# Optimization experiments

Hardware: AMD Instinct MI355X
Metric: run time of the kernel (lower is better)

The kernel has to match this reference:

```python
import jax, jax.numpy as jnp
import numpy as np

B, T, C, H = 2, 2048, 1024, 16
HD = C // H  # 64

def setup_inputs() -> dict:
    key = jax.random.key(0)
    ks = jax.random.split(key, 9)
    s = 0.02
    return {
        "x": jax.random.normal(ks[0], (B, T, C), jnp.float32),
        "Wq": jax.random.normal(ks[1], (C, C), jnp.float32) * s,
        "bq": jax.random.normal(ks[2], (C,), jnp.float32) * s,
        "Wk": jax.random.normal(ks[3], (C, C), jnp.float32) * s,
        "bk": jax.random.normal(ks[4], (C,), jnp.float32) * s,
        "Wv": jax.random.normal(ks[5], (C, C), jnp.float32) * s,
        "bv": jax.random.normal(ks[6], (C,), jnp.float32) * s,
        "Wp": jax.random.normal(ks[7], (C, C), jnp.float32) * s,
        "bp": jax.random.normal(ks[8], (C,), jnp.float32) * s,
    }

def reference(x, Wq, bq, Wk, bk, Wv, bv, Wp, bp):
    Bb, Tt, Cc = x.shape
    hd = Cc // H
    # project and split heads: [B, H, T, hd]
    def heads(W, b):
        return (x @ W.T + b).reshape(Bb, Tt, H, hd).transpose(0, 2, 1, 3)
    q, k, v = heads(Wq, bq), heads(Wk, bk), heads(Wv, bv)
    scale = 1.0 / np.sqrt(hd).astype(np.float32)
    att = jnp.einsum('bhqd,bhkd->bhqk', q, k) * scale
    causal = jnp.tril(jnp.ones((Tt, Tt), bool))
    att = jnp.where(causal[None, None], att, -jnp.inf)
    att = jax.nn.softmax(att, axis=-1)
    y = jnp.einsum('bhqk,bhkd->bhqd', att, v)
    y = y.transpose(0, 2, 1, 3).reshape(Bb, Tt, Cc)
    return y @ Wp.T + bp
```

## Files before the change

### kernel.cpp

```cpp
#include <hip/hip_runtime.h>
#include <hip/hip_bf16.h>

#define Tsz 2048
#define Csz 1024
#define Hn 16

typedef short s8v __attribute__((ext_vector_type(8)));
typedef short s4v __attribute__((ext_vector_type(4)));
typedef float f4v __attribute__((ext_vector_type(4)));

#define QSCALE (0.125f * 1.44269504088896f)

__device__ __forceinline__ short bf_bits(float x) {
    __hip_bfloat16 t = __float2bfloat16(x);
    return *reinterpret_cast<short*>(&t);
}

__device__ __forceinline__ void gload_lds(const void* g, void* l) {
    __builtin_amdgcn_global_load_lds(
        (const __attribute__((address_space(1))) void*)g,
        (__attribute__((address_space(3))) void*)l, 16, 0, 0);
}

__global__ void cvt5(const float* __restrict__ x, const float* __restrict__ wq,
                     const float* __restrict__ wk, const float* __restrict__ wv,
                     const float* __restrict__ wp,
                     short* __restrict__ xo, short* __restrict__ qo,
                     short* __restrict__ ko, short* __restrict__ vo,
                     short* __restrict__ po) {
    const int y = blockIdx.y;
    const float* in; short* out; int n;
    switch (y) {
        case 0: in = x;  out = xo; n = 2 * Tsz * Csz; break;
        case 1: in = wq; out = qo; n = Csz * Csz; break;
        case 2: in = wk; out = ko; n = Csz * Csz; break;
        case 3: in = wv; out = vo; n = Csz * Csz; break;
        default: in = wp; out = po; n = Csz * Csz; break;
    }
    int i = (blockIdx.x * blockDim.x + threadIdx.x) * 4;
    if (i >= n) return;
    float4 v = *(const float4*)(in + i);
    short4 o;
    o.x = bf_bits(v.x); o.y = bf_bits(v.y); o.z = bf_bits(v.z); o.w = bf_bits(v.w);
    *(short4*)(out + i) = o;
}

__global__ __launch_bounds__(256, 2) void qkv_gemm(
    const short* __restrict__ X,
    const short* __restrict__ Wq, const short* __restrict__ Wk, const short* __restrict__ Wv,
    const float* __restrict__ bq, const float* __restrict__ bk, const float* __restrict__ bv,
    short* __restrict__ Qo, short* __restrict__ Ko, short* __restrict__ Vto)
{
    const int z = blockIdx.z;
    const short* W = (z == 0) ? Wq : (z == 1) ? Wk : Wv;
    const float* bias = (z == 0) ? bq : (z == 1) ? bk : bv;

    __shared__ __align__(16) short Ash[128 * 32];
    __shared__ __align__(16) short Bsh[128 * 32];

    const int tid = threadIdx.x, lane = tid & 63, wave = tid >> 6;
    const int ln = lane & 15, hi = lane >> 4;
    const int m0 = blockIdx.x * 128, n0 = blockIdx.y * 128;
    const int wm = (wave >> 1) * 64, wn = (wave & 1) * 64;

    const short* Ag = X + (size_t)(m0 + (tid >> 2)) * Csz + (tid & 3) * 8;
    const short* Bg = W + (size_t)(n0 + (tid >> 2)) * Csz + (tid & 3) * 8;

    f4v acc[4][4];
    #pragma unroll
    for (int mt = 0; mt < 4; mt++)
        #pragma unroll
        for (int nt = 0; nt < 4; nt++)
            #pragma unroll
            for (int i = 0; i < 4; i++) acc[mt][nt][i] = 0.f;

    for (int k0 = 0; k0 < Csz; k0 += 32) {
        __syncthreads();
        gload_lds(Ag + k0, Ash + tid * 8);
        gload_lds(Ag + k0 + (size_t)64 * Csz, Ash + 2048 + tid * 8);
        gload_lds(Bg + k0, Bsh + tid * 8);
        gload_lds(Bg + k0 + (size_t)64 * Csz, Bsh + 2048 + tid * 8);
        __syncthreads();

        s8v af[4], bfr[4];
        #pragma unroll
        for (int mt = 0; mt < 4; mt++)
            af[mt] = *(const s8v*)(Ash + (wm + mt * 16 + ln) * 32 + hi * 8);
        #pragma unroll
        for (int nt = 0; nt < 4; nt++)
            bfr[nt] = *(const s8v*)(Bsh + (wn + nt * 16 + ln) * 32 + hi * 8);
        #pragma unroll
        for (int mt = 0; mt < 4; mt++)
            #pragma unroll
            for (int nt = 0; nt < 4; nt++)
                acc[mt][nt] = __builtin_amdgcn_mfma_f32_16x16x32_bf16(af[mt], bfr[nt], acc[mt][nt], 0, 0, 0);
    }

    const float scale = (z == 0) ? QSCALE : 1.0f;
    short* out = (z == 0) ? Qo : Ko;

    #pragma unroll
    for (int nt = 0; nt < 4; nt++) {
        const int col = n0 + wn + nt * 16 + ln;
        const float bvv = bias[col];
        #pragma unroll
        for (int mt = 0; mt < 4; mt++) {
            const int row0 = m0 + wm + mt * 16 + hi * 4;
            if (z == 2) {
                const int b = row0 >> 11, t = row0 & 2047;
                s4v pk;
                #pragma unroll
                for (int i = 0; i < 4; i++) pk[i] = bf_bits(acc[mt][nt][i] + bvv);
                *(s4v*)(Vto + (size_t)(b * 1024 + col) * Tsz + t) = pk;
            } else {
                #pragma unroll
                for (int i = 0; i < 4; i++)
                    out[(size_t)(row0 + i) * Csz + col] = bf_bits((acc[mt][nt][i] + bvv) * scale);
            }
        }
    }
}

__global__ __launch_bounds__(256, 2) void proj_gemm(
    const short* __restrict__ A, const short* __restrict__ W,
    const float* __restrict__ bias, float* __restrict__ out)
{
    __shared__ __align__(16) short Ash[128 * 32];
    __shared__ __align__(16) short Bsh[128 * 32];

    const int tid = threadIdx.x, lane = tid & 63, wave = tid >> 6;
    const int ln = lane & 15, hi = lane >> 4;
    const int m0 = blockIdx.x * 128, n0 = blockIdx.y * 128;
    const int wm = (wave >> 1) * 64, wn = (wave & 1) * 64;

    const short* Ag = A + (size_t)(m0 + (tid >> 2)) * Csz + (tid & 3) * 8;
    const short* Bg = W + (size_t)(n0 + (tid >> 2)) * Csz + (tid & 3) * 8;

    f4v acc[4][4];
    #pragma unroll
    for (int mt = 0; mt < 4; mt++)
        #pragma unroll
        for (int nt = 0; nt < 4; nt++)
            #pragma unroll
            for (int i = 0; i < 4; i++) acc[mt][nt][i] = 0.f;

    for (int k0 = 0; k0 < Csz; k0 += 32) {
        __syncthreads();
        gload_lds(Ag + k0, Ash + tid * 8);
        gload_lds(Ag + k0 + (size_t)64 * Csz, Ash + 2048 + tid * 8);
        gload_lds(Bg + k0, Bsh + tid * 8);
        gload_lds(Bg + k0 + (size_t)64 * Csz, Bsh + 2048 + tid * 8);
        __syncthreads();

        s8v af[4], bfr[4];
        #pragma unroll
        for (int mt = 0; mt < 4; mt++)
            af[mt] = *(const s8v*)(Ash + (wm + mt * 16 + ln) * 32 + hi * 8);
        #pragma unroll
        for (int nt = 0; nt < 4; nt++)
            bfr[nt] = *(const s8v*)(Bsh + (wn + nt * 16 + ln) * 32 + hi * 8);
        #pragma unroll
        for (int mt = 0; mt < 4; mt++)
            #pragma unroll
            for (int nt = 0; nt < 4; nt++)
                acc[mt][nt] = __builtin_amdgcn_mfma_f32_16x16x32_bf16(af[mt], bfr[nt], acc[mt][nt], 0, 0, 0);
    }

    #pragma unroll
    for (int nt = 0; nt < 4; nt++) {
        const int col = n0 + wn + nt * 16 + ln;
        const float bvv = bias[col];
        #pragma unroll
        for (int mt = 0; mt < 4; mt++)
            #pragma unroll
            for (int i = 0; i < 4; i++)
                out[(size_t)(m0 + wm + mt * 16 + hi * 4 + i) * Csz + col] = acc[mt][nt][i] + bvv;
    }
}

__global__ __launch_bounds__(256, 2) void attn4(
    const short* __restrict__ Q, const short* __restrict__ Kg,
    const short* __restrict__ Vt, short* __restrict__ Y)
{
    __shared__ __align__(16) short Ksh[64 * 72];
    __shared__ __align__(16) short Vsh[64 * 72];
    __shared__ __align__(16) short Psh[4][16 * 72];

    const int tid = threadIdx.x, lane = tid & 63, wave = tid >> 6;
    const int ln = lane & 15, hi = lane >> 4;
    const int p = blockIdx.x;
    const int qts[2] = { p, 31 - p };
    const int bh = blockIdx.y;
    const size_t base = (size_t)(bh >> 4) * Tsz * Csz + (size_t)(bh & 15) * 64;
    const size_t vtbase = (size_t)bh * 64 * Tsz;
    const int qrel = wave * 16 + ln;
    short* Pq = Psh[wave];

    s8v qf[2][2];
    #pragma unroll
    for (int t = 0; t < 2; t++)
        #pragma unroll
        for (int kk = 0; kk < 2; kk++)
            qf[t][kk] = *(const s8v*)(Q + base + (size_t)(qts[t] * 64 + qrel) * Csz + kk * 32 + hi * 8);

    f4v o[2][4], lacc[2];
    #pragma unroll
    for (int t = 0; t < 2; t++) {
        #pragma unroll
        for (int i = 0; i < 4; i++) lacc[t][i] = 0.f;
        #pragma unroll
        for (int dt = 0; dt < 4; dt++)
            #pragma unroll
            for (int i = 0; i < 4; i++) o[t][dt][i] = 0.f;
    }

    s8v ones;
    #pragma unroll
    for (int j = 0; j < 8; j++) ones[j] = (short)0x3F80;

    const int sr = tid >> 2, sc = (tid & 3) * 16;
    const short* Kp = Kg + base + (size_t)sr * Csz + sc;
    const short* Vp = Vt + vtbase + (size_t)sr * Tsz + sc;
    short* KshW = Ksh + sr * 72 + sc;
    short* VshW = Vsh + sr * 72 + sc;

    const int nkb = qts[1] + 1;
    for (int kb = 0; kb < nkb; kb++) {
        const int k0 = kb * 64;
        const s8v ka = *(const s8v*)(Kp + (size_t)k0 * Csz);
        const s8v kb2 = *(const s8v*)(Kp + (size_t)k0 * Csz + 8);
        const s8v va = *(const s8v*)(Vp + k0);
        const s8v vb2 = *(const s8v*)(Vp + k0 + 8);
        __syncthreads();
        *(s8v*)(KshW) = ka; *(s8v*)(KshW + 8) = kb2;
        *(s8v*)(VshW) = va; *(s8v*)(VshW + 8) = vb2;
        __syncthreads();

        s8v kf[2][4], vf[2][4];
        #pragma unroll
        for (int nt = 0; nt < 4; nt++)
            #pragma unroll
            for (int kk = 0; kk < 2; kk++) {
                kf[kk][nt] = *(const s8v*)(Ksh + (nt * 16 + ln) * 72 + kk * 32 + hi * 8);
                vf[kk][nt] = *(const s8v*)(Vsh + (nt * 16 + ln) * 72 + kk * 32 + hi * 8);
            }

        #pragma unroll
        for (int t = 0; t < 2; t++) {
            if (t == 0 && kb > qts[0]) continue;
            const bool dg = (kb == qts[t]);

            f4v s[4];
            #pragma unroll
            for (int nt = 0; nt < 4; nt++) {
                #pragma unroll
                for (int i = 0; i < 4; i++) s[nt][i] = 0.f;
                s[nt] = __builtin_amdgcn_mfma_f32_16x16x32_bf16(kf[0][nt], qf[t][0], s[nt], 0, 0, 0);
                s[nt] = __builtin_amdgcn_mfma_f32_16x16x32_bf16(kf[1][nt], qf[t][1], s[nt], 0, 0, 0);
            }

            #pragma unroll
            for (int nt = 0; nt < 4; nt++) {
                float pv[4];
                #pragma unroll
                for (int i = 0; i < 4; i++) pv[i] = exp2f(s[nt][i]);
                if (dg) {
                    const int kr = nt * 16 + hi * 4;
                    #pragma unroll
                    for (int i = 0; i < 4; i++)
                        if (kr + i > qrel) pv[i] = 0.f;
                }
                s4v w;
                #pragma unroll
                for (int i = 0; i < 4; i++) w[i] = bf_bits(pv[i]);
                *(s4v*)(Pq + ln * 72 + nt * 16 + hi * 4) = w;
            }
            const s8v pb0 = *(const s8v*)(Pq + ln * 72 + hi * 8);
            const s8v pb1 = *(const s8v*)(Pq + ln * 72 + 32 + hi * 8);

            #pragma unroll
            for (int dt = 0; dt < 4; dt++) {
                o[t][dt] = __builtin_amdgcn_mfma_f32_16x16x32_bf16(vf[0][dt], pb0, o[t][dt], 0, 0, 0);
                o[t][dt] = __builtin_amdgcn_mfma_f32_16x16x32_bf16(vf[1][dt], pb1, o[t][dt], 0, 0, 0);
            }
            lacc[t] = __builtin_amdgcn_mfma_f32_16x16x32_bf16(ones, pb0, lacc[t], 0, 0, 0);
            lacc[t] = __builtin_amdgcn_mfma_f32_16x16x32_bf16(ones, pb1, lacc[t], 0, 0, 0);
        }
    }

    #pragma unroll
    for (int t = 0; t < 2; t++) {
        const float inv = 1.0f / lacc[t][0];
        const int qrow = qts[t] * 64 + qrel;
        #pragma unroll
        for (int dt = 0; dt < 4; dt++) {
            s4v w;
            #pragma unroll
            for (int i = 0; i < 4; i++) w[i] = bf_bits(o[t][dt][i] * inv);
            *(s4v*)(Y + base + (size_t)qrow * Csz + dt * 16 + hi * 4) = w;
        }
    }
}

extern "C" void kernel_launch(void* const* d_in, const int* in_sizes, int n_in,
                              void* d_out, int out_size, void* d_ws, size_t ws_size,
                              hipStream_t stream) {
    const float* x  = (const float*)d_in[0];
    const float* Wq = (const float*)d_in[1];
    const float* bq = (const float*)d_in[2];
    const float* Wk = (const float*)d_in[3];
    const float* bk = (const float*)d_in[4];
    const float* Wv = (const float*)d_in[5];
    const float* bv = (const float*)d_in[6];
    const float* Wp = (const float*)d_in[7];
    const float* bp = (const float*)d_in[8];

    char* ws = (char*)d_ws;
    short* Xb  = (short*)(ws);
    short* Wqb = (short*)(ws + (8u  << 20));
    short* Wkb = (short*)(ws + (10u << 20));
    short* Wvb = (short*)(ws + (12u << 20));
    short* Wpb = (short*)(ws + (14u << 20));
    short* Qb  = (short*)(ws + (16u << 20));
    short* Kb  = (short*)(ws + (24u << 20));
    short* Vtb = (short*)(ws + (32u << 20));
    short* Yb  = (short*)(ws + (40u << 20));

    hipLaunchKernelGGL(cvt5, dim3(4096, 5), dim3(256), 0, stream,
                       x, Wq, Wk, Wv, Wp, Xb, Wqb, Wkb, Wvb, Wpb);

    hipLaunchKernelGGL(qkv_gemm, dim3(32, 8, 3), dim3(256), 0, stream,
                       Xb, Wqb, Wkb, Wvb, bq, bk, bv, Qb, Kb, Vtb);

    hipLaunchKernelGGL(attn4, dim3(16, 32), dim3(256), 0, stream, Qb, Kb, Vtb, Yb);

    hipLaunchKernelGGL(proj_gemm, dim3(32, 8), dim3(256), 0, stream, Yb, Wpb, bp, (float*)d_out);
}
```

Baseline: 190.4 us.

## Coalesce V-transpose stores, prefetch K/V in attention, shrink proj tiles

The QKV GEMM now stages its V output through an LDS transpose buffer so the transposed V is written as wide coalesced 16-element runs instead of scattered 4-element stores. Its launch bound is raised to 3 blocks per CU. The attention kernel register-prefetches the next K/V tile while computing the current one. It also replaces the row-sum MFMAs against a ones vector with scalar accumulation plus cross-lane shuffles. The projection GEMM uses 128x64 tiles to double the grid for better CU fill, which costs more A reloads and extra LDS and register pressure.

```diff
diff --git a/kernel.cpp b/kernel.cpp
--- a/kernel.cpp
+++ b/kernel.cpp
@@ -45,7 +45,7 @@
     *(short4*)(out + i) = o;
 }
 
-__global__ __launch_bounds__(256, 2) void qkv_gemm(
+__global__ __launch_bounds__(256, 3) void qkv_gemm(
     const short* __restrict__ X,
     const short* __restrict__ Wq, const short* __restrict__ Wk, const short* __restrict__ Wv,
     const float* __restrict__ bq, const float* __restrict__ bk, const float* __restrict__ bv,
@@ -57,6 +57,7 @@
 
     __shared__ __align__(16) short Ash[128 * 32];
     __shared__ __align__(16) short Bsh[128 * 32];
+    __shared__ __align__(16) short TR[64 * 72];
 
     const int tid = threadIdx.x, lane = tid & 63, wave = tid >> 6;
     const int ln = lane & 15, hi = lane >> 4;
@@ -96,6 +97,37 @@
                 acc[mt][nt] = __builtin_amdgcn_mfma_f32_16x16x32_bf16(af[mt], bfr[nt], acc[mt][nt], 0, 0, 0);
     }
 
+    if (z == 2) {
+        const int b = m0 >> 11, t0 = m0 & 2047;
+        float bvv[4];
+        #pragma unroll
+        for (int nt = 0; nt < 4; nt++) bvv[nt] = bias[n0 + wn + nt * 16 + ln];
+        #pragma unroll
+        for (int ph = 0; ph < 4; ph++) {
+            const int mh = ph >> 1, nh = ph & 1;
+            __syncthreads();
+            if ((wave >> 1) == mh && (wave & 1) == nh) {
+                #pragma unroll
+                for (int mt = 0; mt < 4; mt++)
+                    #pragma unroll
+                    for (int nt = 0; nt < 4; nt++) {
+                        s4v pk;
+                        #pragma unroll
+                        for (int i = 0; i < 4; i++) pk[i] = bf_bits(acc[mt][nt][i] + bvv[nt]);
+                        *(s4v*)(TR + (nt * 16 + ln) * 72 + mt * 16 + hi * 4) = pk;
+                    }
+            }
+            __syncthreads();
+            const int chl = tid >> 2, seg = tid & 3;
+            const s8v r0 = *(const s8v*)(TR + chl * 72 + seg * 16);
+            const s8v r1 = *(const s8v*)(TR + chl * 72 + seg * 16 + 8);
+            short* dst = Vto + (size_t)(b * 1024 + n0 + nh * 64 + chl) * Tsz + t0 + mh * 64 + seg * 16;
+            *(s8v*)(dst) = r0;
+            *(s8v*)(dst + 8) = r1;
+        }
+        return;
+    }
+
     const float scale = (z == 0) ? QSCALE : 1.0f;
     short* out = (z == 0) ? Qo : Ko;
 
@@ -106,17 +138,9 @@
         #pragma unroll
         for (int mt = 0; mt < 4; mt++) {
             const int row0 = m0 + wm + mt * 16 + hi * 4;
-            if (z == 2) {
-                const int b = row0 >> 11, t = row0 & 2047;
-                s4v pk;
-                #pragma unroll
-                for (int i = 0; i < 4; i++) pk[i] = bf_bits(acc[mt][nt][i] + bvv);
-                *(s4v*)(Vto + (size_t)(b * 1024 + col) * Tsz + t) = pk;
-            } else {
-                #pragma unroll
-                for (int i = 0; i < 4; i++)
-                    out[(size_t)(row0 + i) * Csz + col] = bf_bits((acc[mt][nt][i] + bvv) * scale);
-            }
+            #pragma unroll
+            for (int i = 0; i < 4; i++)
+                out[(size_t)(row0 + i) * Csz + col] = bf_bits((acc[mt][nt][i] + bvv) * scale);
         }
     }
 }
@@ -126,21 +150,21 @@
     const float* __restrict__ bias, float* __restrict__ out)
 {
     __shared__ __align__(16) short Ash[128 * 32];
-    __shared__ __align__(16) short Bsh[128 * 32];
+    __shared__ __align__(16) short Bsh[64 * 32];
 
     const int tid = threadIdx.x, lane = tid & 63, wave = tid >> 6;
     const int ln = lane & 15, hi = lane >> 4;
-    const int m0 = blockIdx.x * 128, n0 = blockIdx.y * 128;
-    const int wm = (wave >> 1) * 64, wn = (wave & 1) * 64;
+    const int m0 = blockIdx.x * 128, n0 = blockIdx.y * 64;
+    const int wm = (wave >> 1) * 64, wn = (wave & 1) * 32;
 
     const short* Ag = A + (size_t)(m0 + (tid >> 2)) * Csz + (tid & 3) * 8;
     const short* Bg = W + (size_t)(n0 + (tid >> 2)) * Csz + (tid & 3) * 8;
 
-    f4v acc[4][4];
+    f4v acc[4][2];
     #pragma unroll
     for (int mt = 0; mt < 4; mt++)
         #pragma unroll
-        for (int nt = 0; nt < 4; nt++)
+        for (int nt = 0; nt < 2; nt++)
             #pragma unroll
             for (int i = 0; i < 4; i++) acc[mt][nt][i] = 0.f;
 
@@ -149,25 +173,24 @@
         gload_lds(Ag + k0, Ash + tid * 8);
         gload_lds(Ag + k0 + (size_t)64 * Csz, Ash + 2048 + tid * 8);
         gload_lds(Bg + k0, Bsh + tid * 8);
-        gload_lds(Bg + k0 + (size_t)64 * Csz, Bsh + 2048 + tid * 8);
-        __syncthreads();
-
-        s8v af[4], bfr[4];
+        __syncthreads();
+
+        s8v af[4], bfr[2];
         #pragma unroll
         for (int mt = 0; mt < 4; mt++)
             af[mt] = *(const s8v*)(Ash + (wm + mt * 16 + ln) * 32 + hi * 8);
         #pragma unroll
-        for (int nt = 0; nt < 4; nt++)
+        for (int nt = 0; nt < 2; nt++)
             bfr[nt] = *(const s8v*)(Bsh + (wn + nt * 16 + ln) * 32 + hi * 8);
         #pragma unroll
         for (int mt = 0; mt < 4; mt++)
             #pragma unroll
-            for (int nt = 0; nt < 4; nt++)
+            for (int nt = 0; nt < 2; nt++)
                 acc[mt][nt] = __builtin_amdgcn_mfma_f32_16x16x32_bf16(af[mt], bfr[nt], acc[mt][nt], 0, 0, 0);
     }
 
     #pragma unroll
-    for (int nt = 0; nt < 4; nt++) {
+    for (int nt = 0; nt < 2; nt++) {
         const int col = n0 + wn + nt * 16 + ln;
         const float bvv = bias[col];
         #pragma unroll
@@ -178,7 +201,7 @@
     }
 }
 
-__global__ __launch_bounds__(256, 2) void attn4(
+__global__ __launch_bounds__(256, 2) void attn6(
     const short* __restrict__ Q, const short* __restrict__ Kg,
     const short* __restrict__ Vt, short* __restrict__ Y)
 {
@@ -203,20 +226,14 @@
         for (int kk = 0; kk < 2; kk++)
             qf[t][kk] = *(const s8v*)(Q + base + (size_t)(qts[t] * 64 + qrel) * Csz + kk * 32 + hi * 8);
 
-    f4v o[2][4], lacc[2];
-    #pragma unroll
-    for (int t = 0; t < 2; t++) {
-        #pragma unroll
-        for (int i = 0; i < 4; i++) lacc[t][i] = 0.f;
+    f4v o[2][4];
+    float lsum[2] = {0.f, 0.f};
+    #pragma unroll
+    for (int t = 0; t < 2; t++)
         #pragma unroll
         for (int dt = 0; dt < 4; dt++)
             #pragma unroll
             for (int i = 0; i < 4; i++) o[t][dt][i] = 0.f;
-    }
-
-    s8v ones;
-    #pragma unroll
-    for (int j = 0; j < 8; j++) ones[j] = (short)0x3F80;
 
     const int sr = tid >> 2, sc = (tid & 3) * 16;
     const short* Kp = Kg + base + (size_t)sr * Csz + sc;
@@ -225,16 +242,22 @@
     short* VshW = Vsh + sr * 72 + sc;
 
     const int nkb = qts[1] + 1;
+    s8v ka  = *(const s8v*)(Kp);
+    s8v kb2 = *(const s8v*)(Kp + 8);
+    s8v va  = *(const s8v*)(Vp);
+    s8v vb2 = *(const s8v*)(Vp + 8);
+
     for (int kb = 0; kb < nkb; kb++) {
-        const int k0 = kb * 64;
-        const s8v ka = *(const s8v*)(Kp + (size_t)k0 * Csz);
-        const s8v kb2 = *(const s8v*)(Kp + (size_t)k0 * Csz + 8);
-        const s8v va = *(const s8v*)(Vp + k0);
-        const s8v vb2 = *(const s8v*)(Vp + k0 + 8);
         __syncthreads();
         *(s8v*)(KshW) = ka; *(s8v*)(KshW + 8) = kb2;
         *(s8v*)(VshW) = va; *(s8v*)(VshW + 8) = vb2;
         __syncthreads();
+
+        const int knx = (kb + 1 < nkb) ? (kb + 1) * 64 : kb * 64;
+        ka  = *(const s8v*)(Kp + (size_t)knx * Csz);
+        kb2 = *(const s8v*)(Kp + (size_t)knx * Csz + 8);
+        va  = *(const s8v*)(Vp + knx);
+        vb2 = *(const s8v*)(Vp + knx + 8);
 
         s8v kf[2][4], vf[2][4];
         #pragma unroll
@@ -270,6 +293,7 @@
                     for (int i = 0; i < 4; i++)
                         if (kr + i > qrel) pv[i] = 0.f;
                 }
+                lsum[t] += (pv[0] + pv[1]) + (pv[2] + pv[3]);
                 s4v w;
                 #pragma unroll
                 for (int i = 0; i < 4; i++) w[i] = bf_bits(pv[i]);
@@ -283,14 +307,15 @@
                 o[t][dt] = __builtin_amdgcn_mfma_f32_16x16x32_bf16(vf[0][dt], pb0, o[t][dt], 0, 0, 0);
                 o[t][dt] = __builtin_amdgcn_mfma_f32_16x16x32_bf16(vf[1][dt], pb1, o[t][dt], 0, 0, 0);
             }
-            lacc[t] = __builtin_amdgcn_mfma_f32_16x16x32_bf16(ones, pb0, lacc[t], 0, 0, 0);
-            lacc[t] = __builtin_amdgcn_mfma_f32_16x16x32_bf16(ones, pb1, lacc[t], 0, 0, 0);
         }
     }
 
     #pragma unroll
     for (int t = 0; t < 2; t++) {
-        const float inv = 1.0f / lacc[t][0];
+        float l = lsum[t];
+        l += __shfl_xor(l, 16);
+        l += __shfl_xor(l, 32);
+        const float inv = 1.0f / l;
         const int qrow = qts[t] * 64 + qrel;
         #pragma unroll
         for (int dt = 0; dt < 4; dt++) {
@@ -332,7 +357,7 @@
     hipLaunchKernelGGL(qkv_gemm, dim3(32, 8, 3), dim3(256), 0, stream,
                        Xb, Wqb, Wkb, Wvb, bq, bk, bv, Qb, Kb, Vtb);
 
-    hipLaunchKernelGGL(attn4, dim3(16, 32), dim3(256), 0, stream, Qb, Kb, Vtb, Yb);
-
-    hipLaunchKernelGGL(proj_gemm, dim3(32, 8), dim3(256), 0, stream, Yb, Wpb, bp, (float*)d_out);
-}
+    hipLaunchKernelGGL(attn6, dim3(16, 32), dim3(256), 0, stream, Qb, Kb, Vtb, Yb);
+
+    hipLaunchKernelGGL(proj_gemm, dim3(32, 16), dim3(256), 0, stream, Yb, Wpb, bp, (float*)d_out);
+}
```

Result: no change. 192.3 us (+1.0%).
